# Performance work log

Measured on AMD Instinct MI355X. Metric: run time of the kernel, lower is better.

## Reference

```python
import jax, jax.numpy as jnp
import numpy as np

B, N, T, D, NEMB = 16, 64, 50, 4, 128  # batch, nodes, timesteps, in-dims, embed
EPS = 1e-20


def setup_inputs() -> dict:
    key = jax.random.key(0)
    ks = jax.random.split(key, 5)
    x = jax.random.normal(ks[0], (B, N, T, D), dtype=jnp.float32)
    # fully-connected directed graph without self loops: E = N*(N-1)
    send_idx, rec_idx = np.where(~np.eye(N, dtype=bool))
    eye = np.eye(N, dtype=np.float32)
    rel_send = jnp.asarray(eye[send_idx])  # [E, N] one-hot
    rel_rec = jnp.asarray(eye[rec_idx])    # [E, N] one-hot
    W_conv = jax.random.normal(ks[1], (D, NEMB), dtype=jnp.float32) / np.sqrt(D)
    b_conv = jax.random.normal(ks[2], (NEMB,), dtype=jnp.float32) * 0.01
    W_skip = jax.random.normal(ks[3], (D, NEMB), dtype=jnp.float32) / np.sqrt(D)
    b_skip = jax.random.normal(ks[4], (NEMB,), dtype=jnp.float32) * 0.01
    return dict(x=x, rel_rec=rel_rec, rel_send=rel_send,
                W_conv=W_conv, b_conv=b_conv, W_skip=W_skip, b_skip=b_skip)


def reference(x, rel_rec, rel_send, W_conv, b_conv, W_skip, b_skip):
    # gather endpoint features: [B, E, T, D]
    senders = jnp.einsum('en,bntd->betd', rel_send, x)
    receivers = jnp.einsum('en,bntd->betd', rel_rec, x)
    # per-edge inverse distance -> [B, T, E]
    spatial_norm = jnp.linalg.norm(receivers - senders, axis=-1)  # [B, E, T]
    adj_values = (1.0 / (spatial_norm + EPS)).transpose(0, 2, 1)   # [B, T, E]
    # rel_send.T @ diag(w) @ rel_rec, without the O(E^2) diag_embed: [B, T, N, N]
    adj = jnp.einsum('es,bte,er->btsr', rel_send, adj_values, rel_rec)
    # symmetric degree normalization D^{-1/2} A D^{-1/2} (no self loops)
    deg = adj.sum(-1)                      # [B, T, N]
    dinv = (deg + EPS) ** -0.5
    adj_n = dinv[..., :, None] * adj * dinv[..., None, :]
    # graph convolution branch
    xp = jnp.transpose(x, (0, 2, 1, 3))    # [B, T, N, D]
    x_conv = jnp.einsum('btnm,btmd->btnd', adj_n, xp) @ W_conv + b_conv
    x_conv = jnp.transpose(x_conv, (0, 2, 1, 3))  # [B, N, T, NEMB]
    # skip branch
    x_skip = x @ W_skip + b_skip           # [B, N, T, NEMB]
    return jax.nn.selu(jnp.concatenate([x_skip, x_conv], axis=-1))
```

## Files before the change

kernel.cpp:

```cpp
#include <hip/hip_runtime.h>
#include <hip/hip_bf16.h>

#define NB 16
#define NN 64
#define NT 50
#define ND 4
#define NE 128
#define CH 256

__device__ __forceinline__ float bf2f(unsigned short u) {
    union { unsigned int i; float f; } c;
    c.i = ((unsigned int)u) << 16;
    return c.f;
}

__device__ __forceinline__ unsigned short f2bf(float f) {
    union { float f; unsigned int i; } c;
    c.f = f;
    unsigned int x = c.i;
    x += 0x7fffu + ((x >> 16) & 1u);
    return (unsigned short)(x >> 16);
}

__device__ __forceinline__ float selu_f(float v) {
    const float scale = 1.0507009873554805f;
    const float alpha = 1.6732632423543772f;
    return v > 0.0f ? scale * v : scale * alpha * (__expf(v) - 1.0f);
}

__device__ __forceinline__ float4 ld4rt(bool isbf, const void* p, size_t off) {
    if (isbf) {
        const ushort4 v = *(const ushort4*)((const unsigned short*)p + off);
        return make_float4(bf2f(v.x), bf2f(v.y), bf2f(v.z), bf2f(v.w));
    }
    return *(const float4*)((const float*)p + off);
}

__device__ __forceinline__ void st4rt(bool isbf, void* p, size_t off, float4 r) {
    if (isbf) {
        *(ushort4*)((unsigned short*)p + off) =
            make_ushort4(f2bf(r.x), f2bf(r.y), f2bf(r.z), f2bf(r.w));
    } else {
        *(float4*)((float*)p + off) = r;
    }
}

__global__ __launch_bounds__(256) void gcn_kernel(
    const void* __restrict__ x, const void* __restrict__ rel,
    const void* __restrict__ Wc, const void* __restrict__ bc,
    const void* __restrict__ Ws, const void* __restrict__ bs,
    void* __restrict__ out)
{
    const bool isbf = (((const unsigned int*)rel)[0] != 0u);

    const int blk = blockIdx.x;
    const int bt = blk >> 2;
    const int qq = blk & 3;
    const int b = bt / NT;
    const int t = bt - b * NT;
    const int tid = threadIdx.x;

    __shared__ float4 xt[NN];
    __shared__ float4 xsc[NN];
    __shared__ float adjm[NN][NN];
    __shared__ float part[256];
    __shared__ float dinv[NN];
    __shared__ float4 yp[NN][4];
    __shared__ float4 y4[NN];
    __shared__ float4 Wsm[ND * NE / 4];
    __shared__ float4 Wcm[ND * NE / 4];
    __shared__ float4 bsm[NE / 4];
    __shared__ float4 bcm[NE / 4];

    if (tid < 128) {
        Wsm[tid] = ld4rt(isbf, Ws, (size_t)tid * 4);
        Wcm[tid] = ld4rt(isbf, Wc, (size_t)tid * 4);
    } else if (tid < 160) {
        const int i = tid - 128;
        bsm[i] = ld4rt(isbf, bs, (size_t)i * 4);
        bcm[i] = ld4rt(isbf, bc, (size_t)i * 4);
    }
    if (tid < NN) {
        xt[tid] = ld4rt(isbf, x, (((size_t)b * NN + tid) * NT + t) * ND);
    }
    __syncthreads();

    const int n = tid >> 2;
    const int q = tid & 3;
    const float4 xn = xt[n];
    float psum = 0.0f;
#pragma unroll
    for (int i = 0; i < 16; ++i) {
        const int m = (q << 4) + ((i + n) & 15);
        const float4 xm = xt[m];
        const float dx = xn.x - xm.x, dy = xn.y - xm.y;
        const float dz = xn.z - xm.z, dw = xn.w - xm.w;
        const float dist = sqrtf(dx * dx + dy * dy + dz * dz + dw * dw);
        const float v = (m == n) ? 0.0f : 1.0f / (dist + 1e-20f);
        adjm[n][m] = v;
        psum += v;
    }
    part[tid] = psum;
    __syncthreads();

    if (tid < NN) {
        const float deg = part[tid * 4] + part[tid * 4 + 1] +
                          part[tid * 4 + 2] + part[tid * 4 + 3];
        const float di = rsqrtf(deg + 1e-20f);
        dinv[tid] = di;
        const float4 v = xt[tid];
        xsc[tid] = make_float4(v.x * di, v.y * di, v.z * di, v.w * di);
    }
    __syncthreads();

    float4 acc = make_float4(0.f, 0.f, 0.f, 0.f);
#pragma unroll
    for (int i = 0; i < 16; ++i) {
        const int m = (q << 4) + ((i + n) & 15);
        const float w = adjm[n][m];
        const float4 xm = xsc[m];
        acc.x = fmaf(w, xm.x, acc.x);
        acc.y = fmaf(w, xm.y, acc.y);
        acc.z = fmaf(w, xm.z, acc.z);
        acc.w = fmaf(w, xm.w, acc.w);
    }
    yp[n][q] = acc;
    __syncthreads();

    if (tid < NN) {
        const float4 s0 = yp[tid][0], s1 = yp[tid][1];
        const float4 s2 = yp[tid][2], s3 = yp[tid][3];
        const float di = dinv[tid];
        y4[tid] = make_float4((s0.x + s1.x + s2.x + s3.x) * di,
                              (s0.y + s1.y + s2.y + s3.y) * di,
                              (s0.z + s1.z + s2.z + s3.z) * di,
                              (s0.w + s1.w + s2.w + s3.w) * di);
    }
    __syncthreads();

    const int j = tid & 63;
    const bool skipb = j < 32;
    const int jj = j & 31;
    const float4* wb = skipb ? Wsm : Wcm;
    const float4 w0 = wb[jj], w1 = wb[32 + jj], w2 = wb[64 + jj], w3 = wb[96 + jj];
    const float4 bias = skipb ? bsm[jj] : bcm[jj];
    const float4* inb = skipb ? xt : y4;
    const int w = tid >> 6;

#pragma unroll
    for (int rr = 0; rr < 4; ++rr) {
        const int nn = (qq << 4) + (w << 2) + rr;
        const float4 in = inb[nn];
        float4 r = bias;
        r.x = fmaf(in.x, w0.x, fmaf(in.y, w1.x, fmaf(in.z, w2.x, fmaf(in.w, w3.x, r.x))));
        r.y = fmaf(in.x, w0.y, fmaf(in.y, w1.y, fmaf(in.z, w2.y, fmaf(in.w, w3.y, r.y))));
        r.z = fmaf(in.x, w0.z, fmaf(in.y, w1.z, fmaf(in.z, w2.z, fmaf(in.w, w3.z, r.z))));
        r.w = fmaf(in.x, w0.w, fmaf(in.y, w1.w, fmaf(in.z, w2.w, fmaf(in.w, w3.w, r.w))));
        r.x = selu_f(r.x);
        r.y = selu_f(r.y);
        r.z = selu_f(r.z);
        r.w = selu_f(r.w);
        st4rt(isbf, out, (((size_t)b * NN + nn) * NT + t) * CH + 4 * j, r);
    }
}

extern "C" void kernel_launch(void* const* d_in, const int* in_sizes, int n_in,
                              void* d_out, int out_size, void* d_ws, size_t ws_size,
                              hipStream_t stream) {
    const void* x   = d_in[0];
    const void* rel = d_in[1];
    const void* Wc  = d_in[3];
    const void* bc  = d_in[4];
    const void* Ws  = d_in[5];
    const void* bs  = d_in[6];
    gcn_kernel<<<dim3(NB * NT * 4), dim3(256), 0, stream>>>(x, rel, Wc, bc, Ws, bs, d_out);
}
```

Baseline: 102.6 us.

## Split GCN into adjacency phase and row-contiguous projection phase via workspace

```diff
diff --git a/kernel.cpp b/kernel.cpp
--- a/kernel.cpp
+++ b/kernel.cpp
@@ -45,17 +45,12 @@
     }
 }
 
-__global__ __launch_bounds__(256) void gcn_kernel(
+__global__ __launch_bounds__(256) void gcn_phase1(
     const void* __restrict__ x, const void* __restrict__ rel,
-    const void* __restrict__ Wc, const void* __restrict__ bc,
-    const void* __restrict__ Ws, const void* __restrict__ bs,
-    void* __restrict__ out)
+    float4* __restrict__ ws_y)
 {
     const bool isbf = (((const unsigned int*)rel)[0] != 0u);
-
-    const int blk = blockIdx.x;
-    const int bt = blk >> 2;
-    const int qq = blk & 3;
+    const int bt = blockIdx.x;
     const int b = bt / NT;
     const int t = bt - b * NT;
     const int tid = threadIdx.x;
@@ -66,20 +61,7 @@
     __shared__ float part[256];
     __shared__ float dinv[NN];
     __shared__ float4 yp[NN][4];
-    __shared__ float4 y4[NN];
-    __shared__ float4 Wsm[ND * NE / 4];
-    __shared__ float4 Wcm[ND * NE / 4];
-    __shared__ float4 bsm[NE / 4];
-    __shared__ float4 bcm[NE / 4];
 
-    if (tid < 128) {
-        Wsm[tid] = ld4rt(isbf, Ws, (size_t)tid * 4);
-        Wcm[tid] = ld4rt(isbf, Wc, (size_t)tid * 4);
-    } else if (tid < 160) {
-        const int i = tid - 128;
-        bsm[i] = ld4rt(isbf, bs, (size_t)i * 4);
-        bcm[i] = ld4rt(isbf, bc, (size_t)i * 4);
-    }
     if (tid < NN) {
         xt[tid] = ld4rt(isbf, x, (((size_t)b * NN + tid) * NT + t) * ND);
     }
@@ -131,36 +113,55 @@
         const float4 s0 = yp[tid][0], s1 = yp[tid][1];
         const float4 s2 = yp[tid][2], s3 = yp[tid][3];
         const float di = dinv[tid];
-        y4[tid] = make_float4((s0.x + s1.x + s2.x + s3.x) * di,
-                              (s0.y + s1.y + s2.y + s3.y) * di,
-                              (s0.z + s1.z + s2.z + s3.z) * di,
-                              (s0.w + s1.w + s2.w + s3.w) * di);
+        ws_y[(size_t)bt * NN + tid] =
+            make_float4((s0.x + s1.x + s2.x + s3.x) * di,
+                        (s0.y + s1.y + s2.y + s3.y) * di,
+                        (s0.z + s1.z + s2.z + s3.z) * di,
+                        (s0.w + s1.w + s2.w + s3.w) * di);
     }
-    __syncthreads();
+}
 
+__global__ __launch_bounds__(256) void gcn_phase2(
+    const void* __restrict__ x, const void* __restrict__ rel,
+    const float4* __restrict__ ws_y,
+    const void* __restrict__ Wc, const void* __restrict__ bc,
+    const void* __restrict__ Ws, const void* __restrict__ bs,
+    void* __restrict__ out)
+{
+    const bool isbf = (((const unsigned int*)rel)[0] != 0u);
+    const int tid = threadIdx.x;
     const int j = tid & 63;
+    const int g = blockIdx.x * 4 + (tid >> 6);
+
     const bool skipb = j < 32;
     const int jj = j & 31;
-    const float4* wb = skipb ? Wsm : Wcm;
-    const float4 w0 = wb[jj], w1 = wb[32 + jj], w2 = wb[64 + jj], w3 = wb[96 + jj];
-    const float4 bias = skipb ? bsm[jj] : bcm[jj];
-    const float4* inb = skipb ? xt : y4;
-    const int w = tid >> 6;
+    const void* wsrc = skipb ? Ws : Wc;
+    const float4 w0 = ld4rt(isbf, wsrc, 0 * NE + 4 * jj);
+    const float4 w1 = ld4rt(isbf, wsrc, 1 * NE + 4 * jj);
+    const float4 w2 = ld4rt(isbf, wsrc, 2 * NE + 4 * jj);
+    const float4 w3 = ld4rt(isbf, wsrc, 3 * NE + 4 * jj);
+    const float4 bias = ld4rt(isbf, skipb ? bs : bc, 4 * jj);
 
 #pragma unroll
-    for (int rr = 0; rr < 4; ++rr) {
-        const int nn = (qq << 4) + (w << 2) + rr;
-        const float4 in = inb[nn];
-        float4 r = bias;
-        r.x = fmaf(in.x, w0.x, fmaf(in.y, w1.x, fmaf(in.z, w2.x, fmaf(in.w, w3.x, r.x))));
-        r.y = fmaf(in.x, w0.y, fmaf(in.y, w1.y, fmaf(in.z, w2.y, fmaf(in.w, w3.y, r.y))));
-        r.z = fmaf(in.x, w0.z, fmaf(in.y, w1.z, fmaf(in.z, w2.z, fmaf(in.w, w3.z, r.z))));
-        r.w = fmaf(in.x, w0.w, fmaf(in.y, w1.w, fmaf(in.z, w2.w, fmaf(in.w, w3.w, r.w))));
-        r.x = selu_f(r.x);
-        r.y = selu_f(r.y);
-        r.z = selu_f(r.z);
-        r.w = selu_f(r.w);
-        st4rt(isbf, out, (((size_t)b * NN + nn) * NT + t) * CH + 4 * j, r);
+    for (int r = 0; r < 4; ++r) {
+        const int row = g * 4 + r;
+        const int b = row / (NN * NT);
+        const int rem = row - b * (NN * NT);
+        const int n = rem / NT;
+        const int t = rem - n * NT;
+        const float4 in = skipb
+            ? ld4rt(isbf, x, (size_t)row * ND)
+            : ws_y[((size_t)b * NT + t) * NN + n];
+        float4 v = bias;
+        v.x = fmaf(in.x, w0.x, fmaf(in.y, w1.x, fmaf(in.z, w2.x, fmaf(in.w, w3.x, v.x))));
+        v.y = fmaf(in.x, w0.y, fmaf(in.y, w1.y, fmaf(in.z, w2.y, fmaf(in.w, w3.y, v.y))));
+        v.z = fmaf(in.x, w0.z, fmaf(in.y, w1.z, fmaf(in.z, w2.z, fmaf(in.w, w3.z, v.z))));
+        v.w = fmaf(in.x, w0.w, fmaf(in.y, w1.w, fmaf(in.z, w2.w, fmaf(in.w, w3.w, v.w))));
+        v.x = selu_f(v.x);
+        v.y = selu_f(v.y);
+        v.z = selu_f(v.z);
+        v.w = selu_f(v.w);
+        st4rt(isbf, out, (size_t)row * CH + 4 * j, v);
     }
 }
 
@@ -173,5 +174,9 @@
     const void* bc  = d_in[4];
     const void* Ws  = d_in[5];
     const void* bs  = d_in[6];
-    gcn_kernel<<<dim3(NB * NT * 4), dim3(256), 0, stream>>>(x, rel, Wc, bc, Ws, bs, d_out);
+    float4* ws_y = (float4*)d_ws;
+
+    gcn_phase1<<<dim3(NB * NT), dim3(256), 0, stream>>>(x, rel, ws_y);
+    gcn_phase2<<<dim3(NB * NT * NN / 16), dim3(256), 0, stream>>>(
+        x, rel, ws_y, Wc, bc, Ws, bs, d_out);
 }
```

Measured after the change: 97.60 us. 4.9% less time.
